# Performance work log

Hardware: AMD Instinct MI355X
Metric: run time of the kernel (lower is better)

The kernel has to match this reference:

```python
import jax, jax.numpy as jnp
import numpy as np
import math

D_MODEL = 1024
NHEAD = 16
FACTOR = 1
B, L = 2, 4096


def setup_inputs() -> dict:
    key = jax.random.key(0)
    ks = jax.random.split(key, 12)
    s = 0.02
    inp = {
        "query": jax.random.normal(ks[0], (B, L, D_MODEL), dtype=jnp.float32),
        "key": jax.random.normal(ks[1], (B, L, D_MODEL), dtype=jnp.float32),
        "value": jax.random.normal(ks[2], (B, L, D_MODEL), dtype=jnp.float32),
        "Wq": jax.random.normal(ks[3], (D_MODEL, D_MODEL), dtype=jnp.float32) * s,
        "bq": jnp.zeros((D_MODEL,), dtype=jnp.float32),
        "Wk": jax.random.normal(ks[4], (D_MODEL, D_MODEL), dtype=jnp.float32) * s,
        "bk": jnp.zeros((D_MODEL,), dtype=jnp.float32),
        "Wv": jax.random.normal(ks[5], (D_MODEL, D_MODEL), dtype=jnp.float32) * s,
        "bv": jnp.zeros((D_MODEL,), dtype=jnp.float32),
        "Wo": jax.random.normal(ks[6], (D_MODEL, D_MODEL), dtype=jnp.float32) * s,
        "bo": jnp.zeros((D_MODEL,), dtype=jnp.float32),
    }
    return inp


def _autocorr_forward(query, key, value, Wq, bq, Wk, bk, Wv, bv, Wo, bo):
    Bq, Lq, d = query.shape
    Lk = key.shape[1]
    H = NHEAD
    Dk = d // H

    # projections, split heads -> (B, H, L, Dk)
    Q = (query @ Wq + bq).reshape(Bq, Lq, H, Dk).transpose(0, 2, 1, 3)
    K = (key @ Wk + bk).reshape(Bq, Lk, H, Dk).transpose(0, 2, 1, 3)
    V = (value @ Wv + bv).reshape(Bq, Lk, H, Dk).transpose(0, 2, 1, 3)

    # align K/V sequence length to L_q (truncate or zero-pad)
    if Lk > Lq:
        K = K[:, :, :Lq, :]
        V = V[:, :, :Lq, :]
    elif Lq > Lk:
        pad = [(0, 0), (0, 0), (0, Lq - Lk), (0, 0)]
        K = jnp.pad(K, pad)
        V = jnp.pad(V, pad)
    Lloc = Lq

    # FFT-based circular autocorrelation along the sequence axis
    Qf = jnp.fft.rfft(Q, axis=2)
    Kf = jnp.fft.rfft(K, axis=2)
    corr = jnp.fft.irfft(Qf * jnp.conj(Kf), n=Lloc, axis=2)  # (B,H,L,Dk)
    corr_mean = corr.mean(axis=-1)  # (B,H,L)

    top_k = min(max(1, int(FACTOR * math.log(Lloc + 1))), Lloc)
    w, idx = jax.lax.top_k(corr_mean, top_k)  # (B,H,k)
    w = jax.nn.softmax(w, axis=-1)

    # circular gather of V at each delay, weighted combine over top-k delays
    ar = jnp.arange(Lloc)
    shifted = (ar[None, None, None, :] + idx[..., None]) % Lloc  # (B,H,k,L)
    rolled = jnp.take_along_axis(
        V[:, :, None, :, :], shifted[..., None], axis=3
    )  # (B,H,k,L,Dk)
    out = jnp.einsum("bhk,bhkld->bhld", w, rolled)  # (B,H,L,Dk)

    out = out.transpose(0, 2, 1, 3).reshape(Bq, Lq, d)
    return out @ Wo + bo  # dropout is identity in eval mode


def reference(query, key, value, Wq, bq, Wk, bk, Wv, bv, Wo, bo):
    return _autocorr_forward(query, key, value, Wq, bq, Wk, bk, Wv, bv, Wo, bo)
```

## Files before the change

### kernel.cpp

```cpp
#include <hip/hip_runtime.h>
#include <hip/hip_bf16.h>

#define LL 4096
#define NH 16
#define DM 1024
#define DK 64
#define MTOT 8192
#define PI_F 3.14159265358979323846f

typedef short short8 __attribute__((ext_vector_type(8)));
typedef float f32x4 __attribute__((ext_vector_type(4)));

typedef __attribute__((address_space(1))) const unsigned char g_u8;
typedef __attribute__((address_space(3))) unsigned char l_u8;

__device__ __forceinline__ void gload16(const void* g, void* l){
  __builtin_amdgcn_global_load_lds((g_u8*)g, (l_u8*)l, 16, 0, 0);
}

__device__ __forceinline__ unsigned short f2bf(float x){
  union { float f; unsigned int u; } v; v.f = x;
  unsigned int r = v.u + 0x7FFFu + ((v.u >> 16) & 1u);
  return (unsigned short)(r >> 16);
}
__device__ __forceinline__ float bf2f(unsigned short u){
  union { unsigned int u; float f; } v; v.u = ((unsigned int)u) << 16; return v.f;
}

__global__ void k_conv_x(const float* __restrict__ in, unsigned short* __restrict__ out, int n4){
  int i = blockIdx.x*256 + threadIdx.x;
  if (i >= n4) return;
  float4 v = ((const float4*)in)[i];
  ushort4 o; o.x=f2bf(v.x); o.y=f2bf(v.y); o.z=f2bf(v.z); o.w=f2bf(v.w);
  ((ushort4*)out)[i] = o;
}

__global__ void k_conv_x_split2(const float* __restrict__ q, const float* __restrict__ k,
                                unsigned short* __restrict__ hi, unsigned short* __restrict__ lo, int n4){
  int i = blockIdx.x*256 + threadIdx.x;
  float4 v = (i < n4) ? ((const float4*)q)[i] : ((const float4*)k)[i - n4];
  ushort4 oh, ol;
  oh.x=f2bf(v.x); ol.x=f2bf(v.x - bf2f(oh.x));
  oh.y=f2bf(v.y); ol.y=f2bf(v.y - bf2f(oh.y));
  oh.z=f2bf(v.z); ol.z=f2bf(v.z - bf2f(oh.z));
  oh.w=f2bf(v.w); ol.w=f2bf(v.w - bf2f(oh.w));
  ((ushort4*)hi)[i] = oh;
  ((ushort4*)lo)[i] = ol;
}

__global__ void k_conv_wt(const float* __restrict__ W0, const float* __restrict__ W1,
                          const float* __restrict__ W2, const float* __restrict__ W3,
                          unsigned short* __restrict__ hi_base, unsigned short* __restrict__ lo_base){
  const float* W = (blockIdx.z==0)?W0:(blockIdx.z==1)?W1:(blockIdx.z==2)?W2:W3;
  unsigned short* oh = hi_base + (size_t)blockIdx.z*DM*DM;
  unsigned short* ol = (blockIdx.z<2) ? (lo_base + (size_t)blockIdx.z*DM*DM) : nullptr;
  __shared__ unsigned short th[64][65];
  __shared__ unsigned short tl[64][65];
  int n0 = blockIdx.x*64, k0 = blockIdx.y*64;
  for (int i=0;i<16;i++){
    int g = i*256 + threadIdx.x;
    int kr = g>>6, nc = g&63;
    float x = W[(size_t)(k0+kr)*DM + n0+nc];
    unsigned short h = f2bf(x);
    th[kr][nc] = h;
    tl[kr][nc] = f2bf(x - bf2f(h));
  }
  __syncthreads();
  for (int i=0;i<16;i++){
    int g = i*256 + threadIdx.x;
    int nr = g>>6, kc = g&63;
    oh[(size_t)(n0+nr)*DM + k0+kc] = th[kc][nr];
    if (ol) ol[(size_t)(n0+nr)*DM + k0+kc] = tl[kc][nr];
  }
}

template<int MODE>
__global__ __launch_bounds__(256) void k_gemm_plain(
    const short* __restrict__ A, const short* __restrict__ Bt,
    const float* __restrict__ bias, float* __restrict__ Cf, unsigned short* __restrict__ Cb)
{
  __shared__ short As[128][64];
  __shared__ short Bs[128][64];
  const int m0 = blockIdx.x*128, n0 = blockIdx.y*128;
  const int tid = threadIdx.x;
  const int wave = tid>>6, lane = tid&63;
  const int wm = (wave>>1)*64, wn = (wave&1)*64;
  const int li = lane&15, lk4 = lane>>4;
  const int srow = lane>>3;
  const int scol = (((lane&7) ^ srow))*8;
  f32x4 acc[4][4] = {};
  for (int kt=0; kt<16; ++kt){
    #pragma unroll
    for (int c=0;c<4;c++){
      int q = wave*4+c;
      int row = q*8 + srow;
      gload16(&A [(size_t)(m0+row)*DM + kt*64 + scol], &As[q*8][0]);
      gload16(&Bt[(size_t)(n0+row)*DM + kt*64 + scol], &Bs[q*8][0]);
    }
    __syncthreads();
    #pragma unroll
    for (int kk=0; kk<64; kk+=32){
      short8 af[4], bfv[4];
      #pragma unroll
      for (int mi=0;mi<4;mi++)
        af[mi] = *(const short8*)&As[wm+mi*16+li][((( (kk>>3)+lk4 ) ^ (li&7)))*8];
      #pragma unroll
      for (int ni=0;ni<4;ni++)
        bfv[ni] = *(const short8*)&Bs[wn+ni*16+li][((( (kk>>3)+lk4 ) ^ (li&7)))*8];
      #pragma unroll
      for (int mi=0;mi<4;mi++)
        #pragma unroll
        for (int ni=0;ni<4;ni++)
          acc[mi][ni] = __builtin_amdgcn_mfma_f32_16x16x32_bf16(af[mi], bfv[ni], acc[mi][ni], 0,0,0);
    }
    __syncthreads();
  }
  #pragma unroll
  for (int mi=0;mi<4;mi++){
    #pragma unroll
    for (int ni=0;ni<4;ni++){
      const int col = n0 + wn + ni*16 + li;
      const float bv = bias[col];
      const int mbase = m0 + wm + mi*16 + lk4*4;
      #pragma unroll
      for (int r=0;r<4;r++){
        const int row = mbase + r;
        float v = acc[mi][ni][r] + bv;
        if (MODE==2){
          Cf[(size_t)row*DM + col] = v;
        } else {
          int b = row>>12, l = row&(LL-1), h = col>>6, d = col&63;
          Cb[(((size_t)(b*NH+h))*LL + l)*DK + d] = f2bf(v);
        }
      }
    }
  }
}

__global__ __launch_bounds__(512, 2) void k_gemm_split256(
    const short* __restrict__ Ahi, const short* __restrict__ Alo,
    const short* __restrict__ Whi, const short* __restrict__ Wlo,
    const float* __restrict__ bias_q, const float* __restrict__ bias_k,
    float* __restrict__ OutQ, float* __restrict__ OutK, int nq)
{
  __shared__ short AsH[2][256][32];
  __shared__ short AsL[2][256][32];
  __shared__ short BsH[2][256][32];
  __shared__ short BsL[2][256][32];

  const int side = (blockIdx.x >= nq) ? 1 : 0;
  const int m0 = blockIdx.x*256, n0 = blockIdx.y*256;
  const short* Bhi = Whi + (size_t)side*DM*DM;
  const short* Blo = Wlo + (size_t)side*DM*DM;
  const float* bias = side ? bias_k : bias_q;
  float* Ct = side ? OutK : OutQ;
  const int ml0 = m0 - side*(nq*256);

  const int tid = threadIdx.x;
  const int wave = tid>>6, lane = tid&63;
  const int wm = (wave>>2)*128;
  const int wn = (wave&3)*64;
  const int li = lane&15, lk4 = lane>>4;

  const int sr = lane>>2, sc4 = lane&3;
  const int scol = ((sc4 ^ (sr&3) ^ ((sr>>2)&3)))*8;
  const int rbyte = ((lk4 ^ (li&3) ^ (li>>2)))*8;

  f32x4 acc[8][4] = {};

  auto STAGE_HALF = [&](int kt, int bufi, int h){
    const int r0 = h*128 + wave*16;
    const int gr = r0 + sr;
    const int kof = kt*32 + scol;
    gload16(&Ahi[(size_t)(m0+gr)*DM + kof], &AsH[bufi][r0][0]);
    gload16(&Alo[(size_t)(m0+gr)*DM + kof], &AsL[bufi][r0][0]);
    gload16(&Bhi[(size_t)(n0+gr)*DM + kof], &BsH[bufi][r0][0]);
    gload16(&Blo[(size_t)(n0+gr)*DM + kof], &BsL[bufi][r0][0]);
  };

  STAGE_HALF(0, 0, 0);
  STAGE_HALF(0, 0, 1);

  for (int kt=0; kt<32; ++kt){
    const int cur = kt&1;
    if (kt < 31){
      STAGE_HALF(kt+1, cur^1, 0);
      asm volatile("s_waitcnt vmcnt(4)" ::: "memory");
    } else {
      asm volatile("s_waitcnt vmcnt(0)" ::: "memory");
    }
    asm volatile("" ::: "memory");
    __builtin_amdgcn_s_barrier();
    asm volatile("" ::: "memory");

    short8 bhf[4], blf[4];
    #pragma unroll
    for (int ni=0;ni<4;ni++){
      bhf[ni] = *(const short8*)&BsH[cur][wn+ni*16+li][rbyte];
      blf[ni] = *(const short8*)&BsL[cur][wn+ni*16+li][rbyte];
    }
    #pragma unroll
    for (int p=0;p<4;p++){
      if (p==2 && kt<31) STAGE_HALF(kt+1, cur^1, 1);
      short8 ah0 = *(const short8*)&AsH[cur][wm+(2*p  )*16+li][rbyte];
      short8 al0 = *(const short8*)&AsL[cur][wm+(2*p  )*16+li][rbyte];
      short8 ah1 = *(const short8*)&AsH[cur][wm+(2*p+1)*16+li][rbyte];
      short8 al1 = *(const short8*)&AsL[cur][wm+(2*p+1)*16+li][rbyte];
      __builtin_amdgcn_s_setprio(1);
      #pragma unroll
      for (int ni=0;ni<4;ni++){
        f32x4 a0 = acc[2*p][ni];
        a0 = __builtin_amdgcn_mfma_f32_16x16x32_bf16(ah0, bhf[ni], a0, 0,0,0);
        a0 = __builtin_amdgcn_mfma_f32_16x16x32_bf16(ah0, blf[ni], a0, 0,0,0);
        a0 = __builtin_amdgcn_mfma_f32_16x16x32_bf16(al0, bhf[ni], a0, 0,0,0);
        acc[2*p][ni] = a0;
        f32x4 a1 = acc[2*p+1][ni];
        a1 = __builtin_amdgcn_mfma_f32_16x16x32_bf16(ah1, bhf[ni], a1, 0,0,0);
        a1 = __builtin_amdgcn_mfma_f32_16x16x32_bf16(ah1, blf[ni], a1, 0,0,0);
        a1 = __builtin_amdgcn_mfma_f32_16x16x32_bf16(al1, bhf[ni], a1, 0,0,0);
        acc[2*p+1][ni] = a1;
      }
      __builtin_amdgcn_s_setprio(0);
    }
    asm volatile("" ::: "memory");
    __builtin_amdgcn_s_barrier();
    asm volatile("" ::: "memory");
  }

  #pragma unroll
  for (int mi=0;mi<8;mi++){
    #pragma unroll
    for (int ni=0;ni<4;ni++){
      const int col = n0 + wn + ni*16 + li;
      const float bv = bias[col];
      const int mbase = ml0 + wm + mi*16 + lk4*4;
      const int b = mbase>>12, l0 = mbase&(LL-1);
      const int h = col>>6, d = col&63;
      float4 o;
      o.x = acc[mi][ni][0]+bv; o.y = acc[mi][ni][1]+bv;
      o.z = acc[mi][ni][2]+bv; o.w = acc[mi][ni][3]+bv;
      *(float4*)&Ct[(((size_t)(b*NH+h))*DK + d)*LL + l0] = o;
    }
  }
}

__device__ __forceinline__ float2 cmul(float2 a, float2 b){
  return make_float2(a.x*b.x - a.y*b.y, a.x*b.y + a.y*b.x);
}
__device__ __forceinline__ int swz(int i){ return i ^ ((i>>4)&15); }

__device__ __forceinline__ float2 ctw(float2 v, int k, float sgn){
  float c, s;
  switch(k){
    case 0: return v;
    case 1: c= 0.92387953251f; s= 0.38268343236f; break;
    case 2: c= 0.70710678119f; s= 0.70710678119f; break;
    case 3: c= 0.38268343236f; s= 0.92387953251f; break;
    case 4: c= 0.f;            s= 1.f;            break;
    case 6: c=-0.70710678119f; s= 0.70710678119f; break;
    default:c=-0.92387953251f; s=-0.38268343236f; break;
  }
  s *= sgn;
  return make_float2(v.x*c - v.y*s, v.x*s + v.y*c);
}

template<int SGN>
__device__ __forceinline__ void dft16(float2 x[16]){
  const float sg = (float)SGN;
  #pragma unroll
  for (int m1=0;m1<4;m1++){
    float2 a=x[m1], b=x[m1+4], c=x[m1+8], d=x[m1+12];
    float acx=a.x+c.x, acy=a.y+c.y, sx=a.x-c.x, sy=a.y-c.y;
    float bdx=b.x+d.x, bdy=b.y+d.y, tx=b.x-d.x, ty=b.y-d.y;
    float ix=-sg*ty, iy=sg*tx;
    x[m1]    = make_float2(acx+bdx, acy+bdy);
    x[m1+4]  = make_float2(sx+ix,  sy+iy);
    x[m1+8]  = make_float2(acx-bdx, acy-bdy);
    x[m1+12] = make_float2(sx-ix,  sy-iy);
  }
  float2 y[16];
  #pragma unroll
  for (int p1=0;p1<4;p1++){
    float2 a = x[4*p1+0];
    float2 b = ctw(x[4*p1+1], p1,   sg);
    float2 c = ctw(x[4*p1+2], 2*p1, sg);
    float2 d = ctw(x[4*p1+3], 3*p1, sg);
    float acx=a.x+c.x, acy=a.y+c.y, sx=a.x-c.x, sy=a.y-c.y;
    float bdx=b.x+d.x, bdy=b.y+d.y, tx=b.x-d.x, ty=b.y-d.y;
    float ix=-sg*ty, iy=sg*tx;
    y[p1]    = make_float2(acx+bdx, acy+bdy);
    y[p1+4]  = make_float2(sx+ix,  sy+iy);
    y[p1+8]  = make_float2(acx-bdx, acy-bdy);
    y[p1+12] = make_float2(sx-ix,  sy-iy);
  }
  #pragma unroll
  for (int i=0;i<16;i++) x[i]=y[i];
}

template<int SGN>
__device__ __forceinline__ void twiddle_apply(float2 x[16], int j, float invden){
  float th = (float)SGN * 6.28318530717958647f * (float)j * invden;
  float s, c; __sincosf(th, &s, &c);
  float2 w1 = make_float2(c, s);
  float2 w2 = cmul(w1,w1), w3 = cmul(w2,w1), w4 = cmul(w2,w2);
  float2 w8 = cmul(w4,w4), w12 = cmul(w8,w4);
  float2 wl[4] = {make_float2(1.f,0.f), w1, w2, w3};
  float2 wh[4] = {make_float2(1.f,0.f), w4, w8, w12};
  #pragma unroll
  for (int m=1;m<16;m++){
    float2 tw = cmul(wh[m>>2], wl[m&3]);
    x[m] = cmul(x[m], tw);
  }
}

template<int SGN>
__device__ __forceinline__ void fft_stages(float2* lds, float2 x[16], int t){
  dft16<SGN>(x);
  #pragma unroll
  for (int p=0;p<16;p++) lds[swz(t*16+p)] = x[p];
  __syncthreads();
  #pragma unroll
  for (int m=0;m<16;m++) x[m] = lds[swz(t + 256*m)];
  __syncthreads();
  twiddle_apply<SGN>(x, t&15, 1.0f/256.0f);
  dft16<SGN>(x);
  {
    int base = (t>>4)*256 + (t&15);
    #pragma unroll
    for (int p=0;p<16;p++) lds[swz(base + 16*p)] = x[p];
  }
  __syncthreads();
  #pragma unroll
  for (int m=0;m<16;m++) x[m] = lds[swz(t + 256*m)];
  __syncthreads();
  twiddle_apply<SGN>(x, t, 1.0f/4096.0f);
  dft16<SGN>(x);
  #pragma unroll
  for (int p=0;p<16;p++) lds[swz(t + 256*p)] = x[p];
  __syncthreads();
}

__global__ __launch_bounds__(256) void k_fft_fwd(const float* __restrict__ Qt, const float* __restrict__ Kt,
                                                 float* __restrict__ Spart){
  __shared__ float2 lds[4096];
  const int bh = blockIdx.x >> 4, g = blockIdx.x & 15;
  const int t = threadIdx.x;
  float2 pacc[16];
  #pragma unroll
  for (int i=0;i<16;i++) pacc[i]=make_float2(0.f,0.f);
  for (int dd=0; dd<4; ++dd){
    const size_t base = ((size_t)bh*DK + g*4 + dd)*LL;
    float2 x[16];
    #pragma unroll
    for (int m=0;m<16;m++){
      int n = t + 256*m;
      x[m] = make_float2(Qt[base+n], Kt[base+n]);
    }
    fft_stages<-1>(lds, x, t);
    #pragma unroll
    for (int i=0;i<16;i++){
      int f = t + 256*i;
      float2 A = lds[swz(f)];
      float2 Bv = lds[swz((LL-f)&(LL-1))];
      float qr = 0.5f*(A.x+Bv.x), qi = 0.5f*(A.y-Bv.y);
      float kr = 0.5f*(A.y+Bv.y), ki = -0.5f*(A.x-Bv.x);
      pacc[i].x += qr*kr + qi*ki;
      pacc[i].y += qi*kr - qr*ki;
    }
    __syncthreads();
  }
  float2* Sp = (float2*)Spart + (size_t)blockIdx.x*LL;
  #pragma unroll
  for (int i=0;i<16;i++) Sp[t + 256*i] = pacc[i];
}

__global__ __launch_bounds__(256) void k_ifft_topk(const float* __restrict__ Spart,
                                                   float* __restrict__ w8, int* __restrict__ idx8){
  __shared__ float2 lds[4096];
  __shared__ float c[4096];
  __shared__ float rv[256];
  __shared__ int   ri[256];
  __shared__ float topv[8];
  __shared__ int   topi[8];
  const int bh = blockIdx.x, t = threadIdx.x;
  float2 x[16];
  #pragma unroll
  for (int m=0;m<16;m++){
    float2 acc = make_float2(0.f,0.f);
    int n = t + 256*m;
    for (int g2=0; g2<16; ++g2){
      float2 v = ((const float2*)Spart)[((size_t)bh*16+g2)*LL + n];
      acc.x += v.x; acc.y += v.y;
    }
    x[m] = acc;
  }
  fft_stages<1>(lds, x, t);
  const float scale = 1.0f/((float)LL * (float)DK);
  #pragma unroll
  for (int m=0;m<16;m++){ int f=t+256*m; c[f] = lds[swz(f)].x * scale; }
  __syncthreads();
  for (int kk=0; kk<8; kk++){
    float bv = -3.4e38f; int bi = 0;
    #pragma unroll
    for (int i=0;i<16;i++){
      int f = t + 256*i;
      float v = c[f];
      if (v > bv || (v == bv && f < bi)) { bv = v; bi = f; }
    }
    rv[t]=bv; ri[t]=bi;
    __syncthreads();
    for (int off=128; off>0; off>>=1){
      if (t < off){
        float ov = rv[t+off]; int oi = ri[t+off];
        if (ov > rv[t] || (ov == rv[t] && oi < ri[t])) { rv[t]=ov; ri[t]=oi; }
      }
      __syncthreads();
    }
    if (t==0){ topv[kk]=rv[0]; topi[kk]=ri[0]; c[ri[0]] = -3.0e38f; }
    __syncthreads();
  }
  if (t==0){
    float m = topv[0];
    float e[8], sum=0.f;
    for (int k=0;k<8;k++){ e[k]=__expf(topv[k]-m); sum+=e[k]; }
    for (int k=0;k<8;k++){ w8[bh*8+k]=e[k]/sum; idx8[bh*8+k]=topi[k]; }
  }
}

__global__ __launch_bounds__(256) void k_gather(const unsigned short* __restrict__ Vh,
                                                const float* __restrict__ w8, const int* __restrict__ idx8,
                                                unsigned short* __restrict__ Ob){
  const int blk = blockIdx.x;
  const int bh = blk >> 6;
  const int l0 = (blk & 63) * 64;
  const int b = bh >> 4, h = bh & 15;
  float w[8]; int ix[8];
  #pragma unroll
  for (int k=0;k<8;k++){ w[k]=w8[bh*8+k]; ix[k]=idx8[bh*8+k]; }
  const int tid = threadIdx.x;
  const int d8 = (tid & 7) * 8;
  const int lrow = tid >> 3;
  #pragma unroll
  for (int it=0; it<2; ++it){
    const int l = l0 + it*32 + lrow;
    float acc[8] = {0,0,0,0,0,0,0,0};
    #pragma unroll
    for (int k=0;k<8;k++){
      const int sl = (l + ix[k]) & (LL-1);
      short8 v = *(const short8*)&Vh[((size_t)bh*LL + sl)*DK + d8];
      const float wk = w[k];
      #pragma unroll
      for (int j=0;j<8;j++)
        acc[j] += wk * bf2f((unsigned short)v[j]);
    }
    short8 o;
    #pragma unroll
    for (int j=0;j<8;j++) o[j] = (short)f2bf(acc[j]);
    *(short8*)&Ob[((size_t)(b*LL + l))*DM + h*DK + d8] = o;
  }
}

extern "C" void kernel_launch(void* const* d_in, const int* in_sizes, int n_in,
                              void* d_out, int out_size, void* d_ws, size_t ws_size,
                              hipStream_t stream) {
  const float* query = (const float*)d_in[0];
  const float* key   = (const float*)d_in[1];
  const float* value = (const float*)d_in[2];
  const float* Wq = (const float*)d_in[3];
  const float* bq = (const float*)d_in[4];
  const float* Wk = (const float*)d_in[5];
  const float* bk = (const float*)d_in[6];
  const float* Wv = (const float*)d_in[7];
  const float* bv = (const float*)d_in[8];
  const float* Wo = (const float*)d_in[9];
  const float* bo = (const float*)d_in[10];
  float* out = (float*)d_out;

  char* ws = (char*)d_ws;
  const int n4 = MTOT*DM/4;
  const size_t MB16 = (size_t)MTOT*DM*2;

  size_t off = 0;
  auto take = [&](size_t b)->char*{ char* p = ws + off; off += (b + 255) & ~(size_t)255; return p; };

  const size_t merged_bytes = 2*(2*MB16) + (size_t)4*DM*DM*2 + (size_t)2*DM*DM*2
                            + 2*((size_t)2*NH*DK*LL*4) + 16384;

  if (ws_size >= merged_bytes) {
    short* Xs_hi = (short*)take(2*MB16);
    short* Xs_lo = (short*)take(2*MB16);
    short* Wth = (short*)take((size_t)4*DM*DM*2);
    short* Wtl = (short*)take((size_t)2*DM*DM*2);
    float* Qt  = (float*)take((size_t)2*NH*DK*LL*4);
    float* Kt  = (float*)take((size_t)2*NH*DK*LL*4);
    float* w8  = (float*)take(32*8*4);
    int*  idx8 = (int*)take(32*8*4);
    float* Spart = (float*)Xs_hi;
    unsigned short* Ob = (unsigned short*)((char*)Xs_hi + MB16);
    unsigned short* Xv = (unsigned short*)Xs_lo;
    unsigned short* Vh = (unsigned short*)((char*)Xs_lo + MB16);

    k_conv_wt<<<dim3(16,16,4),256,0,stream>>>(Wq,Wk,Wv,Wo,(unsigned short*)Wth,(unsigned short*)Wtl);
    k_conv_x_split2<<<2*n4/256,256,0,stream>>>(query,key,(unsigned short*)Xs_hi,(unsigned short*)Xs_lo,n4);
    k_gemm_split256<<<dim3(64,4),512,0,stream>>>(Xs_hi, Xs_lo, Wth, Wtl, bq, bk, Qt, Kt, 32);
    k_conv_x<<<n4/256,256,0,stream>>>(value, Xv, n4);
    k_gemm_plain<1><<<dim3(64,8),256,0,stream>>>((const short*)Xv, Wth + (size_t)2*DM*DM, bv, nullptr, Vh);
    k_fft_fwd<<<512,256,0,stream>>>(Qt, Kt, Spart);
    k_ifft_topk<<<32,256,0,stream>>>(Spart, w8, idx8);
    k_gather<<<2048,256,0,stream>>>(Vh, w8, idx8, Ob);
    k_gemm_plain<2><<<dim3(64,8),256,0,stream>>>((const short*)Ob, Wth + (size_t)3*DM*DM, bo, out, nullptr);
  } else {
    short* Xhi = (short*)take(MB16);
    short* Xlo = (short*)take(MB16);
    short* Wth = (short*)take((size_t)4*DM*DM*2);
    short* Wtl = (short*)take((size_t)2*DM*DM*2);
    float* Qt  = (float*)take((size_t)2*NH*DK*LL*4);
    float* Kt  = (float*)take((size_t)2*NH*DK*LL*4);
    unsigned short* Vh = (unsigned short*)take((size_t)2*NH*LL*DK*2);
    float* w8  = (float*)take(32*8*4);
    int*  idx8 = (int*)take(32*8*4);
    float* Spart = (float*)Xlo;

    k_conv_wt<<<dim3(16,16,4),256,0,stream>>>(Wq,Wk,Wv,Wo,(unsigned short*)Wth,(unsigned short*)Wtl);

    k_conv_x_split2<<<n4/256,256,0,stream>>>(query,query,(unsigned short*)Xhi,(unsigned short*)Xlo,n4);
    k_gemm_split256<<<dim3(32,4),512,0,stream>>>(Xhi, Xlo, Wth, Wtl, bq, bq, Qt, Qt, 32);

    k_conv_x_split2<<<n4/256,256,0,stream>>>(key,key,(unsigned short*)Xhi,(unsigned short*)Xlo,n4);
    k_gemm_split256<<<dim3(32,4),512,0,stream>>>(Xhi, Xlo, Wth + (size_t)DM*DM, Wtl + (size_t)DM*DM,
                                                 bk, bk, Kt, Kt, 32);

    k_conv_x<<<n4/256,256,0,stream>>>(value,(unsigned short*)Xhi,n4);
    k_gemm_plain<1><<<dim3(64,8),256,0,stream>>>(Xhi, Wth + (size_t)2*DM*DM, bv, nullptr, Vh);

    k_fft_fwd<<<512,256,0,stream>>>(Qt, Kt, Spart);
    k_ifft_topk<<<32,256,0,stream>>>(Spart, w8, idx8);
    k_gather<<<2048,256,0,stream>>>(Vh, w8, idx8, (unsigned short*)Xhi);

    k_gemm_plain<2><<<dim3(64,8),256,0,stream>>>(Xhi, Wth + (size_t)3*DM*DM, bo, out, nullptr);
  }
}
```

Before: 248.7 us.

## Double-buffer plain GEMM, fuse input conversions, and widen forward FFT grid

The plain bf16 GEMM now uses two LDS buffers and prefetches the next K tile before computing the current one. The old per-iteration syncthreads pairs become explicit vmcnt waits plus raw barriers. A new workspace tier fuses the query/key split conversion and the value conversion into one kernel launch. The forward FFT grid doubles to 1024 blocks, each handling 2 channels instead of 4, to improve occupancy, and the partial-sum reduction in ifft_topk now reads 32 partials instead of 16. This adds LDS use and doubles the Spart buffer (it now needs 32 partials), and the small-workspace path moves Spart onto Xhi to fit.

```diff
diff --git a/kernel.cpp b/kernel.cpp
--- a/kernel.cpp
+++ b/kernel.cpp
@@ -46,6 +46,27 @@
   oh.w=f2bf(v.w); ol.w=f2bf(v.w - bf2f(oh.w));
   ((ushort4*)hi)[i] = oh;
   ((ushort4*)lo)[i] = ol;
+}
+
+__global__ void k_conv3(const float* __restrict__ q, const float* __restrict__ k,
+                        const float* __restrict__ v,
+                        unsigned short* __restrict__ hi, unsigned short* __restrict__ lo,
+                        unsigned short* __restrict__ vout, int n4){
+  int i = blockIdx.x*256 + threadIdx.x;
+  if (i < 2*n4){
+    float4 x = (i < n4) ? ((const float4*)q)[i] : ((const float4*)k)[i - n4];
+    ushort4 oh, ol;
+    oh.x=f2bf(x.x); ol.x=f2bf(x.x - bf2f(oh.x));
+    oh.y=f2bf(x.y); ol.y=f2bf(x.y - bf2f(oh.y));
+    oh.z=f2bf(x.z); ol.z=f2bf(x.z - bf2f(oh.z));
+    oh.w=f2bf(x.w); ol.w=f2bf(x.w - bf2f(oh.w));
+    ((ushort4*)hi)[i] = oh;
+    ((ushort4*)lo)[i] = ol;
+  } else {
+    float4 x = ((const float4*)v)[i - 2*n4];
+    ushort4 o; o.x=f2bf(x.x); o.y=f2bf(x.y); o.z=f2bf(x.z); o.w=f2bf(x.w);
+    ((ushort4*)vout)[i - 2*n4] = o;
+  }
 }
 
 __global__ void k_conv_wt(const float* __restrict__ W0, const float* __restrict__ W1,
@@ -79,8 +100,8 @@
     const short* __restrict__ A, const short* __restrict__ Bt,
     const float* __restrict__ bias, float* __restrict__ Cf, unsigned short* __restrict__ Cb)
 {
-  __shared__ short As[128][64];
-  __shared__ short Bs[128][64];
+  __shared__ short As[2][128][64];
+  __shared__ short Bs[2][128][64];
   const int m0 = blockIdx.x*128, n0 = blockIdx.y*128;
   const int tid = threadIdx.x;
   const int wave = tid>>6, lane = tid&63;
@@ -88,32 +109,51 @@
   const int li = lane&15, lk4 = lane>>4;
   const int srow = lane>>3;
   const int scol = (((lane&7) ^ srow))*8;
+
   f32x4 acc[4][4] = {};
-  for (int kt=0; kt<16; ++kt){
+
+  auto STAGE = [&](int kt, int bufi){
     #pragma unroll
     for (int c=0;c<4;c++){
       int q = wave*4+c;
       int row = q*8 + srow;
-      gload16(&A [(size_t)(m0+row)*DM + kt*64 + scol], &As[q*8][0]);
-      gload16(&Bt[(size_t)(n0+row)*DM + kt*64 + scol], &Bs[q*8][0]);
-    }
-    __syncthreads();
+      gload16(&A [(size_t)(m0+row)*DM + kt*64 + scol], &As[bufi][q*8][0]);
+      gload16(&Bt[(size_t)(n0+row)*DM + kt*64 + scol], &Bs[bufi][q*8][0]);
+    }
+  };
+
+  STAGE(0, 0);
+
+  for (int kt=0; kt<16; ++kt){
+    const int cur = kt&1;
+    if (kt < 15){
+      STAGE(kt+1, cur^1);
+      asm volatile("s_waitcnt vmcnt(8)" ::: "memory");
+    } else {
+      asm volatile("s_waitcnt vmcnt(0)" ::: "memory");
+    }
+    asm volatile("" ::: "memory");
+    __builtin_amdgcn_s_barrier();
+    asm volatile("" ::: "memory");
+
     #pragma unroll
     for (int kk=0; kk<64; kk+=32){
       short8 af[4], bfv[4];
       #pragma unroll
       for (int mi=0;mi<4;mi++)
-        af[mi] = *(const short8*)&As[wm+mi*16+li][((( (kk>>3)+lk4 ) ^ (li&7)))*8];
+        af[mi] = *(const short8*)&As[cur][wm+mi*16+li][((( (kk>>3)+lk4 ) ^ (li&7)))*8];
       #pragma unroll
       for (int ni=0;ni<4;ni++)
-        bfv[ni] = *(const short8*)&Bs[wn+ni*16+li][((( (kk>>3)+lk4 ) ^ (li&7)))*8];
+        bfv[ni] = *(const short8*)&Bs[cur][wn+ni*16+li][((( (kk>>3)+lk4 ) ^ (li&7)))*8];
       #pragma unroll
       for (int mi=0;mi<4;mi++)
         #pragma unroll
         for (int ni=0;ni<4;ni++)
           acc[mi][ni] = __builtin_amdgcn_mfma_f32_16x16x32_bf16(af[mi], bfv[ni], acc[mi][ni], 0,0,0);
     }
-    __syncthreads();
+    asm volatile("" ::: "memory");
+    __builtin_amdgcn_s_barrier();
+    asm volatile("" ::: "memory");
   }
   #pragma unroll
   for (int mi=0;mi<4;mi++){
@@ -343,13 +383,13 @@
 __global__ __launch_bounds__(256) void k_fft_fwd(const float* __restrict__ Qt, const float* __restrict__ Kt,
                                                  float* __restrict__ Spart){
   __shared__ float2 lds[4096];
-  const int bh = blockIdx.x >> 4, g = blockIdx.x & 15;
+  const int bh = blockIdx.x >> 5, g = blockIdx.x & 31;
   const int t = threadIdx.x;
   float2 pacc[16];
   #pragma unroll
   for (int i=0;i<16;i++) pacc[i]=make_float2(0.f,0.f);
-  for (int dd=0; dd<4; ++dd){
-    const size_t base = ((size_t)bh*DK + g*4 + dd)*LL;
+  for (int dd=0; dd<2; ++dd){
+    const size_t base = ((size_t)bh*DK + g*2 + dd)*LL;
     float2 x[16];
     #pragma unroll
     for (int m=0;m<16;m++){
@@ -388,8 +428,8 @@
   for (int m=0;m<16;m++){
     float2 acc = make_float2(0.f,0.f);
     int n = t + 256*m;
-    for (int g2=0; g2<16; ++g2){
-      float2 v = ((const float2*)Spart)[((size_t)bh*16+g2)*LL + n];
+    for (int g2=0; g2<32; ++g2){
+      float2 v = ((const float2*)Spart)[((size_t)bh*32+g2)*LL + n];
       acc.x += v.x; acc.y += v.y;
     }
     x[m] = acc;
@@ -483,10 +523,34 @@
   size_t off = 0;
   auto take = [&](size_t b)->char*{ char* p = ws + off; off += (b + 255) & ~(size_t)255; return p; };
 
-  const size_t merged_bytes = 2*(2*MB16) + (size_t)4*DM*DM*2 + (size_t)2*DM*DM*2
-                            + 2*((size_t)2*NH*DK*LL*4) + 16384;
-
-  if (ws_size >= merged_bytes) {
+  const size_t tier2_bytes = 2*(2*MB16) + (size_t)4*DM*DM*2 + (size_t)2*DM*DM*2
+                           + 2*((size_t)2*NH*DK*LL*4) + 16384;
+  const size_t tier1_bytes = tier2_bytes + MB16;
+
+  if (ws_size >= tier1_bytes) {
+    short* Xs_hi = (short*)take(2*MB16);
+    short* Xs_lo = (short*)take(2*MB16);
+    unsigned short* Xv = (unsigned short*)take(MB16);
+    short* Wth = (short*)take((size_t)4*DM*DM*2);
+    short* Wtl = (short*)take((size_t)2*DM*DM*2);
+    float* Qt  = (float*)take((size_t)2*NH*DK*LL*4);
+    float* Kt  = (float*)take((size_t)2*NH*DK*LL*4);
+    float* w8  = (float*)take(32*8*4);
+    int*  idx8 = (int*)take(32*8*4);
+    float* Spart = (float*)Xs_hi;
+    unsigned short* Ob = (unsigned short*)((char*)Xs_hi + MB16);
+    unsigned short* Vh = (unsigned short*)((char*)Xs_lo + MB16);
+
+    k_conv_wt<<<dim3(16,16,4),256,0,stream>>>(Wq,Wk,Wv,Wo,(unsigned short*)Wth,(unsigned short*)Wtl);
+    k_conv3<<<3*n4/256,256,0,stream>>>(query,key,value,
+                                       (unsigned short*)Xs_hi,(unsigned short*)Xs_lo,Xv,n4);
+    k_gemm_split256<<<dim3(64,4),512,0,stream>>>(Xs_hi, Xs_lo, Wth, Wtl, bq, bk, Qt, Kt, 32);
+    k_gemm_plain<1><<<dim3(64,8),256,0,stream>>>((const short*)Xv, Wth + (size_t)2*DM*DM, bv, nullptr, Vh);
+    k_fft_fwd<<<1024,256,0,stream>>>(Qt, Kt, Spart);
+    k_ifft_topk<<<32,256,0,stream>>>(Spart, w8, idx8);
+    k_gather<<<2048,256,0,stream>>>(Vh, w8, idx8, Ob);
+    k_gemm_plain<2><<<dim3(64,8),256,0,stream>>>((const short*)Ob, Wth + (size_t)3*DM*DM, bo, out, nullptr);
+  } else if (ws_size >= tier2_bytes) {
     short* Xs_hi = (short*)take(2*MB16);
     short* Xs_lo = (short*)take(2*MB16);
     short* Wth = (short*)take((size_t)4*DM*DM*2);
@@ -505,7 +569,7 @@
     k_gemm_split256<<<dim3(64,4),512,0,stream>>>(Xs_hi, Xs_lo, Wth, Wtl, bq, bk, Qt, Kt, 32);
     k_conv_x<<<n4/256,256,0,stream>>>(value, Xv, n4);
     k_gemm_plain<1><<<dim3(64,8),256,0,stream>>>((const short*)Xv, Wth + (size_t)2*DM*DM, bv, nullptr, Vh);
-    k_fft_fwd<<<512,256,0,stream>>>(Qt, Kt, Spart);
+    k_fft_fwd<<<1024,256,0,stream>>>(Qt, Kt, Spart);
     k_ifft_topk<<<32,256,0,stream>>>(Spart, w8, idx8);
     k_gather<<<2048,256,0,stream>>>(Vh, w8, idx8, Ob);
     k_gemm_plain<2><<<dim3(64,8),256,0,stream>>>((const short*)Ob, Wth + (size_t)3*DM*DM, bo, out, nullptr);
@@ -519,7 +583,7 @@
     unsigned short* Vh = (unsigned short*)take((size_t)2*NH*LL*DK*2);
     float* w8  = (float*)take(32*8*4);
     int*  idx8 = (int*)take(32*8*4);
-    float* Spart = (float*)Xlo;
+    float* Spart = (float*)Xhi;
 
     k_conv_wt<<<dim3(16,16,4),256,0,stream>>>(Wq,Wk,Wv,Wo,(unsigned short*)Wth,(unsigned short*)Wtl);
 
@@ -533,7 +597,7 @@
     k_conv_x<<<n4/256,256,0,stream>>>(value,(unsigned short*)Xhi,n4);
     k_gemm_plain<1><<<dim3(64,8),256,0,stream>>>(Xhi, Wth + (size_t)2*DM*DM, bv, nullptr, Vh);
 
-    k_fft_fwd<<<512,256,0,stream>>>(Qt, Kt, Spart);
+    k_fft_fwd<<<1024,256,0,stream>>>(Qt, Kt, Spart);
     k_ifft_topk<<<32,256,0,stream>>>(Spart, w8, idx8);
     k_gather<<<2048,256,0,stream>>>(Vh, w8, idx8, (unsigned short*)Xhi);
 
```

Measured after the change: 255.7 us. 2.8% more time.
